# Kernel optimization log

Measured on AMD Instinct MI355X. Metric: run time of the kernel, lower is better.

## Reference

```python
import jax, jax.numpy as jnp
import numpy as np

# FP4 E2M1 magnitude lookup table (3-bit magnitude index)
FP4_LUT = jnp.array([0.0, 0.5, 1.0, 1.5, 2.0, 3.0, 4.0, 6.0], dtype=jnp.float32)
E8M0_BIAS = 127


def setup_inputs() -> dict:
    key = jax.random.key(0)
    k_in, k_pw, k_sc, k_b = jax.random.split(key, 4)
    B, S, I, O, BS = 4, 2048, 4096, 11008, 32
    inp = jax.random.normal(k_in, (B, S, I), dtype=jnp.float32)
    # packed MXFP4 codes: two 4-bit codes per byte
    packed_weight = jax.random.randint(k_pw, (O, I // 2), 0, 256, dtype=jnp.int32)
    # E8M0 exponents near the bias so dequantized magnitudes are O(1)
    weight_scales = jax.random.randint(k_sc, (O, I // BS), 118, 132, dtype=jnp.int32)
    bias = jax.random.normal(k_b, (O,), dtype=jnp.float32) * 0.02
    return {"input": inp, "bias": bias, "packed_weight": packed_weight,
            "weight_scales": weight_scales}


def _dequantize_mxfp4(packed_weight, weight_scales):
    O, P = packed_weight.shape
    I = P * 2
    bs = I // weight_scales.shape[1]
    lo = packed_weight & 0xF          # first element of each pair: low nibble
    hi = (packed_weight >> 4) & 0xF   # second element: high nibble
    codes = jnp.stack([lo, hi], axis=-1).reshape(O, I)  # [O, I]
    mag = FP4_LUT[codes & 0x7]
    sign = jnp.where((codes & 0x8) > 0, -1.0, 1.0)
    vals = sign * mag                                   # [O, I] fp4 values
    scale = jnp.exp2((weight_scales - E8M0_BIAS).astype(jnp.float32))  # [O, I/bs]
    w = (vals.reshape(O, I // bs, bs) * scale[:, :, None]).reshape(O, I)
    return w


def reference(input, bias, packed_weight, weight_scales):
    # quantized-inference path: on-the-fly block dequant + F.linear
    w = _dequantize_mxfp4(packed_weight, weight_scales)  # [O, I]
    out = jnp.einsum('bsi,oi->bso', input, w) + bias     # [B, S, O]
    return out
```

## Files before the change

kernel.cpp:

```cpp
#include <hip/hip_runtime.h>
#include <stdint.h>

typedef __attribute__((ext_vector_type(8))) short bf16x8;
typedef __attribute__((ext_vector_type(8))) unsigned short u16x8;
typedef __attribute__((ext_vector_type(4))) float f32x4;
typedef __attribute__((ext_vector_type(4))) int i32x4;

static constexpr int MDIM = 8192;
static constexpr int KDIM = 4096;
static constexpr int NDIM = 11008;
static constexpr int BM = 256, BN = 256, BK = 64;
static constexpr int NBX = NDIM / BN;
static constexpr int NBY = MDIM / BM;


static __device__ __forceinline__ unsigned short f2bf(float f) {
  unsigned int u = __builtin_bit_cast(unsigned int, f);
  return (unsigned short)((u + 0x7FFFu + ((u >> 16) & 1u)) >> 16);
}

static __device__ __forceinline__ float fp4_val(unsigned int c) {
  unsigned int m = c & 1u, e = (c >> 1) & 3u, s = (c >> 3) & 1u;
  unsigned int bits = e ? (((126u + e) << 23) | (m << 22)) : (m ? 0x3F000000u : 0u);
  bits |= s << 31;
  return __builtin_bit_cast(float, bits);
}

static constexpr int CONV_BLOCKS = (MDIM * KDIM / 8) / 256;
static constexpr int DEQ_BLOCKS  = (NDIM * (KDIM / 32)) / 256;

__global__ __launch_bounds__(256) void prep_kernel(
    const float4* __restrict__ in, u16x8* __restrict__ aout,
    const int* __restrict__ pw, const int* __restrict__ sc,
    unsigned short* __restrict__ wout) {
  if (blockIdx.x < CONV_BLOCKS) {
    int i = blockIdx.x * 256 + threadIdx.x;
    float4 v0 = in[2 * (size_t)i];
    float4 v1 = in[2 * (size_t)i + 1];
    u16x8 r;
    r[0] = f2bf(v0.x); r[1] = f2bf(v0.y); r[2] = f2bf(v0.z); r[3] = f2bf(v0.w);
    r[4] = f2bf(v1.x); r[5] = f2bf(v1.y); r[6] = f2bf(v1.z); r[7] = f2bf(v1.w);
    aout[i] = r;
  } else {
    int tid = (blockIdx.x - CONV_BLOCKS) * 256 + threadIdx.x;
    int o = tid >> 7;
    int b = tid & 127;
    const i32x4* src = (const i32x4*)(pw + (size_t)o * (KDIM / 2) + b * 16);
    unsigned int e = (unsigned int)sc[(size_t)o * (KDIM / 32) + b];
    float scale = __builtin_bit_cast(float, e << 23);
    unsigned short* dst = wout + (size_t)o * KDIM + b * 32;
#pragma unroll
    for (int v = 0; v < 4; ++v) {
      i32x4 w4 = src[v];
      u16x8 r;
#pragma unroll
      for (int j = 0; j < 4; ++j) {
        unsigned int w = (unsigned int)w4[j];
        r[2 * j]     = f2bf(fp4_val(w & 0xFu) * scale);
        r[2 * j + 1] = f2bf(fp4_val((w >> 4) & 0xFu) * scale);
      }
      *(u16x8*)(dst + 8 * v) = r;
    }
  }
}


#define GLDS16(gp, lp)                                                                  \
  __builtin_amdgcn_global_load_lds((const __attribute__((address_space(1))) void*)(gp), \
                                   (__attribute__((address_space(3))) void*)(lp), 16, 0, 0)

#define BAR() asm volatile("s_barrier" ::: "memory")

#define MFMA16(ACC, AV, BV, MO)                                                          \
  _Pragma("unroll") for (int m_ = 0; m_ < 4; ++m_)                                       \
  _Pragma("unroll") for (int n_ = 0; n_ < 4; ++n_)                                       \
      ACC[MO + m_][n_] = __builtin_amdgcn_mfma_f32_16x16x32_bf16(AV[m_], BV[n_],         \
                                                                 ACC[MO + m_][n_], 0, 0, 0)

template <int SLOT, bool STAGE>
__device__ __forceinline__ void ktile(
    unsigned char* lds, const unsigned short*& gA, const unsigned short*& gB,
    int stq, int aBase, int bBase, int kof0, int kof1, f32x4 (&acc)[8][4]) {
  const unsigned char* sa = lds + SLOT * 65536;
  const unsigned char* sb = sa + 32768;
  unsigned char* da = lds + (SLOT ^ 1) * 65536 + stq;
  unsigned char* db = da + 32768;
  bf16x8 a[4], b[4], a2[4];

#pragma unroll
  for (int m = 0; m < 4; ++m) a[m] = *(const bf16x8*)(sa + aBase + m * 2048 + kof0);
#pragma unroll
  for (int n = 0; n < 4; ++n) b[n] = *(const bf16x8*)(sb + bBase + n * 2048 + kof0);
  if (STAGE) {
    GLDS16(gB, db);
    GLDS16(gB + (size_t)64 * KDIM, db + 8192);
    asm volatile("s_waitcnt vmcnt(2)" ::: "memory");
  } else {
    asm volatile("s_waitcnt vmcnt(0)" ::: "memory");
  }
  BAR();
  __builtin_amdgcn_s_setprio(1);
  MFMA16(acc, a, b, 0);
  __builtin_amdgcn_s_setprio(0);
  BAR();

#pragma unroll
  for (int m = 0; m < 4; ++m) a2[m] = *(const bf16x8*)(sa + aBase + (4 + m) * 2048 + kof0);
  if (STAGE) {
    GLDS16(gB + (size_t)128 * KDIM, db + 16384);
    GLDS16(gB + (size_t)192 * KDIM, db + 24576);
  }
  BAR();
  __builtin_amdgcn_s_setprio(1);
  MFMA16(acc, a2, b, 4);
  __builtin_amdgcn_s_setprio(0);
  BAR();

#pragma unroll
  for (int m = 0; m < 4; ++m) a[m] = *(const bf16x8*)(sa + aBase + m * 2048 + kof1);
#pragma unroll
  for (int n = 0; n < 4; ++n) b[n] = *(const bf16x8*)(sb + bBase + n * 2048 + kof1);
  if (STAGE) {
    GLDS16(gA, da);
    GLDS16(gA + (size_t)128 * KDIM, da + 16384);
  }
  BAR();
  __builtin_amdgcn_s_setprio(1);
  MFMA16(acc, a, b, 0);
  __builtin_amdgcn_s_setprio(0);
  BAR();

#pragma unroll
  for (int m = 0; m < 4; ++m) a2[m] = *(const bf16x8*)(sa + aBase + (4 + m) * 2048 + kof1);
  if (STAGE) {
    GLDS16(gA + (size_t)64 * KDIM, da + 8192);
    GLDS16(gA + (size_t)192 * KDIM, da + 24576);
    gA += BK; gB += BK;
    asm volatile("s_waitcnt vmcnt(2)" ::: "memory");
  }
  BAR();
  __builtin_amdgcn_s_setprio(1);
  MFMA16(acc, a2, b, 4);
  __builtin_amdgcn_s_setprio(0);
  BAR();
}

__global__ __launch_bounds__(512, 2) void gemm_mx_kernel(
    const unsigned short* __restrict__ A,
    const unsigned short* __restrict__ Bw,
    const float* __restrict__ bias,
    float* __restrict__ C) {
  __shared__ __align__(16) unsigned char lds[2 * 65536];

  const int t = threadIdx.x;
  const int lane = t & 63;
  const int wave = t >> 6;
  const int wr = wave >> 2;
  const int wc = wave & 3;

  const int bid = blockIdx.x;
  const int swb = (bid & 7) * ((NBX * NBY) / 8) + (bid >> 3);
  const int by = swb / NBX;
  const int bx = swb - by * NBX;
  const int m0 = by * BM, n0 = bx * BN;

  const int fl = lane & 15;
  const int fh = lane >> 4;
  const int kof0 = ((fh)     ^ (fl & 7)) * 16;
  const int kof1 = ((4 + fh) ^ (fl & 7)) * 16;
  const int aBase = (wr * 128 + fl) * 128;
  const int bBase = (wc * 64 + fl) * 128;

  const int stq = t * 16;
  const int srow = t >> 3;
  const int koff = 8 * ((t & 7) ^ (srow & 7));
  const unsigned short* gA = A + (size_t)(m0 + srow) * KDIM + koff;
  const unsigned short* gB = Bw + (size_t)(n0 + srow) * KDIM + koff;

  f32x4 acc[8][4] = {};

  {
    unsigned char* da = lds + stq;
    unsigned char* db = da + 32768;
    GLDS16(gB, db);
    GLDS16(gB + (size_t)64 * KDIM, db + 8192);
    GLDS16(gB + (size_t)128 * KDIM, db + 16384);
    GLDS16(gB + (size_t)192 * KDIM, db + 24576);
    GLDS16(gA, da);
    GLDS16(gA + (size_t)128 * KDIM, da + 16384);
    GLDS16(gA + (size_t)64 * KDIM, da + 8192);
    GLDS16(gA + (size_t)192 * KDIM, da + 24576);
    gA += BK; gB += BK;
    asm volatile("s_waitcnt vmcnt(2)" ::: "memory");
    BAR();
  }

  for (int it = 0; it < 31; ++it) {
    ktile<0, true>(lds, gA, gB, stq, aBase, bBase, kof0, kof1, acc);
    ktile<1, true>(lds, gA, gB, stq, aBase, bBase, kof0, kof1, acc);
  }
  ktile<0, true>(lds, gA, gB, stq, aBase, bBase, kof0, kof1, acc);
  ktile<1, false>(lds, gA, gB, stq, aBase, bBase, kof0, kof1, acc);

#pragma unroll
  for (int n = 0; n < 4; ++n) {
    const int gn = n0 + wc * 64 + n * 16 + fl;
    const float bv = bias[gn];
#pragma unroll
    for (int m = 0; m < 8; ++m) {
      const int gm = m0 + wr * 128 + m * 16 + fh * 4;
      float* cp = C + (size_t)gm * NDIM + gn;
#pragma unroll
      for (int r = 0; r < 4; ++r)
        cp[(size_t)r * NDIM] = acc[m][n][r] + bv;
    }
  }
}

extern "C" void kernel_launch(void* const* d_in, const int* in_sizes, int n_in,
                              void* d_out, int out_size, void* d_ws, size_t ws_size,
                              hipStream_t stream) {
  const float* inp  = (const float*)d_in[0];
  const float* bias = (const float*)d_in[1];
  const int* pw     = (const int*)d_in[2];
  const int* sc     = (const int*)d_in[3];
  float* out = (float*)d_out;

  unsigned short* a_bf = (unsigned short*)d_ws;
  unsigned short* w_bf = a_bf + (size_t)MDIM * KDIM;
  size_t need = ((size_t)MDIM * KDIM + (size_t)NDIM * KDIM) * sizeof(unsigned short);
  if (ws_size < need) return;

  prep_kernel<<<dim3(CONV_BLOCKS + DEQ_BLOCKS), dim3(256), 0, stream>>>(
      (const float4*)inp, (u16x8*)a_bf, pw, sc, w_bf);
  gemm_mx_kernel<<<dim3(NBX * NBY), dim3(512), 0, stream>>>(a_bf, w_bf, bias, out);
}
```

Before: 859.7 us.

## Switch GEMM to 32x32x16 MFMA with 4-stage BK=32 LDS pipeline

Replaces the 16x16x32 bf16 MFMA tiling with 32x32x16 MFMAs, giving each wave a 4x2 grid of 32x32 accumulators. The K tile is halved to 32 and the LDS is split into four 32 KB slots, so three tiles are in flight through global_load_lds with a counted vmcnt wait. Each k-tile now needs one barrier instead of several. This aims to cut barrier overhead and hide global-memory latency better. In exchange it adds more pipeline stages with shorter compute per stage and a new swizzle and epilogue mapping that must stay correct.

```diff
diff --git a/kernel.cpp b/kernel.cpp
--- a/kernel.cpp
+++ b/kernel.cpp
@@ -3,13 +3,13 @@
 
 typedef __attribute__((ext_vector_type(8))) short bf16x8;
 typedef __attribute__((ext_vector_type(8))) unsigned short u16x8;
-typedef __attribute__((ext_vector_type(4))) float f32x4;
+typedef __attribute__((ext_vector_type(16))) float f32x16;
 typedef __attribute__((ext_vector_type(4))) int i32x4;
 
 static constexpr int MDIM = 8192;
 static constexpr int KDIM = 4096;
 static constexpr int NDIM = 11008;
-static constexpr int BM = 256, BN = 256, BK = 64;
+static constexpr int BM = 256, BN = 256, BK = 32;
 static constexpr int NBX = NDIM / BN;
 static constexpr int NBY = MDIM / BM;
 
@@ -71,78 +71,47 @@
 
 #define BAR() asm volatile("s_barrier" ::: "memory")
 
-#define MFMA16(ACC, AV, BV, MO)                                                          \
-  _Pragma("unroll") for (int m_ = 0; m_ < 4; ++m_)                                       \
-  _Pragma("unroll") for (int n_ = 0; n_ < 4; ++n_)                                       \
-      ACC[MO + m_][n_] = __builtin_amdgcn_mfma_f32_16x16x32_bf16(AV[m_], BV[n_],         \
-                                                                 ACC[MO + m_][n_], 0, 0, 0)
-
-template <int SLOT, bool STAGE>
+template <int SLOT, bool STAGE, int VN>
 __device__ __forceinline__ void ktile(
     unsigned char* lds, const unsigned short*& gA, const unsigned short*& gB,
-    int stq, int aBase, int bBase, int kof0, int kof1, f32x4 (&acc)[8][4]) {
-  const unsigned char* sa = lds + SLOT * 65536;
-  const unsigned char* sb = sa + 32768;
-  unsigned char* da = lds + (SLOT ^ 1) * 65536 + stq;
-  unsigned char* db = da + 32768;
-  bf16x8 a[4], b[4], a2[4];
-
-#pragma unroll
-  for (int m = 0; m < 4; ++m) a[m] = *(const bf16x8*)(sa + aBase + m * 2048 + kof0);
-#pragma unroll
-  for (int n = 0; n < 4; ++n) b[n] = *(const bf16x8*)(sb + bBase + n * 2048 + kof0);
+    int stq, int aBase, int bBase, int kof0, int kof1, f32x16 (&acc)[4][2]) {
+  if constexpr (VN == 8)      asm volatile("s_waitcnt vmcnt(8)" ::: "memory");
+  else if constexpr (VN == 4) asm volatile("s_waitcnt vmcnt(4)" ::: "memory");
+  else                        asm volatile("s_waitcnt vmcnt(0)" ::: "memory");
+  BAR();
   if (STAGE) {
-    GLDS16(gB, db);
-    GLDS16(gB + (size_t)64 * KDIM, db + 8192);
-    asm volatile("s_waitcnt vmcnt(2)" ::: "memory");
-  } else {
-    asm volatile("s_waitcnt vmcnt(0)" ::: "memory");
-  }
-  BAR();
+    unsigned char* da = lds + ((SLOT + 3) & 3) * 32768 + stq;
+    GLDS16(gA, da);
+    GLDS16(gA + (size_t)128 * KDIM, da + 8192);
+    GLDS16(gB, da + 16384);
+    GLDS16(gB + (size_t)128 * KDIM, da + 24576);
+    gA += BK; gB += BK;
+  }
+  const unsigned char* sa = lds + SLOT * 32768;
+  const unsigned char* sb = sa + 16384;
+  bf16x8 a[4], b[2];
+#pragma unroll
+  for (int mf = 0; mf < 4; ++mf) a[mf] = *(const bf16x8*)(sa + aBase + mf * 2048 + kof0);
+#pragma unroll
+  for (int nf = 0; nf < 2; ++nf) b[nf] = *(const bf16x8*)(sb + bBase + nf * 2048 + kof0);
   __builtin_amdgcn_s_setprio(1);
-  MFMA16(acc, a, b, 0);
+#pragma unroll
+  for (int mf = 0; mf < 4; ++mf)
+#pragma unroll
+    for (int nf = 0; nf < 2; ++nf)
+      acc[mf][nf] = __builtin_amdgcn_mfma_f32_32x32x16_bf16(a[mf], b[nf], acc[mf][nf], 0, 0, 0);
   __builtin_amdgcn_s_setprio(0);
-  BAR();
-
-#pragma unroll
-  for (int m = 0; m < 4; ++m) a2[m] = *(const bf16x8*)(sa + aBase + (4 + m) * 2048 + kof0);
-  if (STAGE) {
-    GLDS16(gB + (size_t)128 * KDIM, db + 16384);
-    GLDS16(gB + (size_t)192 * KDIM, db + 24576);
-  }
-  BAR();
+#pragma unroll
+  for (int mf = 0; mf < 4; ++mf) a[mf] = *(const bf16x8*)(sa + aBase + mf * 2048 + kof1);
+#pragma unroll
+  for (int nf = 0; nf < 2; ++nf) b[nf] = *(const bf16x8*)(sb + bBase + nf * 2048 + kof1);
   __builtin_amdgcn_s_setprio(1);
-  MFMA16(acc, a2, b, 4);
+#pragma unroll
+  for (int mf = 0; mf < 4; ++mf)
+#pragma unroll
+    for (int nf = 0; nf < 2; ++nf)
+      acc[mf][nf] = __builtin_amdgcn_mfma_f32_32x32x16_bf16(a[mf], b[nf], acc[mf][nf], 0, 0, 0);
   __builtin_amdgcn_s_setprio(0);
-  BAR();
-
-#pragma unroll
-  for (int m = 0; m < 4; ++m) a[m] = *(const bf16x8*)(sa + aBase + m * 2048 + kof1);
-#pragma unroll
-  for (int n = 0; n < 4; ++n) b[n] = *(const bf16x8*)(sb + bBase + n * 2048 + kof1);
-  if (STAGE) {
-    GLDS16(gA, da);
-    GLDS16(gA + (size_t)128 * KDIM, da + 16384);
-  }
-  BAR();
-  __builtin_amdgcn_s_setprio(1);
-  MFMA16(acc, a, b, 0);
-  __builtin_amdgcn_s_setprio(0);
-  BAR();
-
-#pragma unroll
-  for (int m = 0; m < 4; ++m) a2[m] = *(const bf16x8*)(sa + aBase + (4 + m) * 2048 + kof1);
-  if (STAGE) {
-    GLDS16(gA + (size_t)64 * KDIM, da + 8192);
-    GLDS16(gA + (size_t)192 * KDIM, da + 24576);
-    gA += BK; gB += BK;
-    asm volatile("s_waitcnt vmcnt(2)" ::: "memory");
-  }
-  BAR();
-  __builtin_amdgcn_s_setprio(1);
-  MFMA16(acc, a2, b, 4);
-  __builtin_amdgcn_s_setprio(0);
-  BAR();
 }
 
 __global__ __launch_bounds__(512, 2) void gemm_mx_kernel(
@@ -150,7 +119,7 @@
     const unsigned short* __restrict__ Bw,
     const float* __restrict__ bias,
     float* __restrict__ C) {
-  __shared__ __align__(16) unsigned char lds[2 * 65536];
+  __shared__ __align__(16) unsigned char lds[4 * 32768];
 
   const int t = threadIdx.x;
   const int lane = t & 63;
@@ -164,55 +133,56 @@
   const int bx = swb - by * NBX;
   const int m0 = by * BM, n0 = bx * BN;
 
-  const int fl = lane & 15;
-  const int fh = lane >> 4;
-  const int kof0 = ((fh)     ^ (fl & 7)) * 16;
-  const int kof1 = ((4 + fh) ^ (fl & 7)) * 16;
-  const int aBase = (wr * 128 + fl) * 128;
-  const int bBase = (wc * 64 + fl) * 128;
+  const int rl = lane & 31;
+  const int hi = lane >> 5;
+  const int kof0 = ((2 * 0 + hi) ^ (rl & 3)) * 16;
+  const int kof1 = ((2 * 1 + hi) ^ (rl & 3)) * 16;
+  const int aBase = (wr * 128 + rl) * 64;
+  const int bBase = (wc * 64 + rl) * 64;
 
   const int stq = t * 16;
-  const int srow = t >> 3;
-  const int koff = 8 * ((t & 7) ^ (srow & 7));
+  const int srow = t >> 2;
+  const int koff = 8 * ((t & 3) ^ (srow & 3));
   const unsigned short* gA = A + (size_t)(m0 + srow) * KDIM + koff;
   const unsigned short* gB = Bw + (size_t)(n0 + srow) * KDIM + koff;
 
-  f32x4 acc[8][4] = {};
-
-  {
-    unsigned char* da = lds + stq;
-    unsigned char* db = da + 32768;
-    GLDS16(gB, db);
-    GLDS16(gB + (size_t)64 * KDIM, db + 8192);
-    GLDS16(gB + (size_t)128 * KDIM, db + 16384);
-    GLDS16(gB + (size_t)192 * KDIM, db + 24576);
+  f32x16 acc[4][2] = {};
+
+#pragma unroll
+  for (int p = 0; p < 3; ++p) {
+    unsigned char* da = lds + p * 32768 + stq;
     GLDS16(gA, da);
-    GLDS16(gA + (size_t)128 * KDIM, da + 16384);
-    GLDS16(gA + (size_t)64 * KDIM, da + 8192);
-    GLDS16(gA + (size_t)192 * KDIM, da + 24576);
+    GLDS16(gA + (size_t)128 * KDIM, da + 8192);
+    GLDS16(gB, da + 16384);
+    GLDS16(gB + (size_t)128 * KDIM, da + 24576);
     gA += BK; gB += BK;
-    asm volatile("s_waitcnt vmcnt(2)" ::: "memory");
-    BAR();
   }
 
   for (int it = 0; it < 31; ++it) {
-    ktile<0, true>(lds, gA, gB, stq, aBase, bBase, kof0, kof1, acc);
-    ktile<1, true>(lds, gA, gB, stq, aBase, bBase, kof0, kof1, acc);
-  }
-  ktile<0, true>(lds, gA, gB, stq, aBase, bBase, kof0, kof1, acc);
-  ktile<1, false>(lds, gA, gB, stq, aBase, bBase, kof0, kof1, acc);
-
-#pragma unroll
-  for (int n = 0; n < 4; ++n) {
-    const int gn = n0 + wc * 64 + n * 16 + fl;
+    ktile<0, true, 8>(lds, gA, gB, stq, aBase, bBase, kof0, kof1, acc);
+    ktile<1, true, 8>(lds, gA, gB, stq, aBase, bBase, kof0, kof1, acc);
+    ktile<2, true, 8>(lds, gA, gB, stq, aBase, bBase, kof0, kof1, acc);
+    ktile<3, true, 8>(lds, gA, gB, stq, aBase, bBase, kof0, kof1, acc);
+  }
+  ktile<0, true, 8>(lds, gA, gB, stq, aBase, bBase, kof0, kof1, acc);
+  ktile<1, false, 8>(lds, gA, gB, stq, aBase, bBase, kof0, kof1, acc);
+  ktile<2, false, 4>(lds, gA, gB, stq, aBase, bBase, kof0, kof1, acc);
+  ktile<3, false, 0>(lds, gA, gB, stq, aBase, bBase, kof0, kof1, acc);
+
+#pragma unroll
+  for (int nf = 0; nf < 2; ++nf) {
+    const int gn = n0 + wc * 64 + nf * 32 + rl;
     const float bv = bias[gn];
 #pragma unroll
-    for (int m = 0; m < 8; ++m) {
-      const int gm = m0 + wr * 128 + m * 16 + fh * 4;
-      float* cp = C + (size_t)gm * NDIM + gn;
-#pragma unroll
-      for (int r = 0; r < 4; ++r)
-        cp[(size_t)r * NDIM] = acc[m][n][r] + bv;
+    for (int mf = 0; mf < 4; ++mf) {
+      const int base = m0 + wr * 128 + mf * 32 + 4 * hi;
+#pragma unroll
+      for (int q = 0; q < 4; ++q) {
+        float* cp = C + (size_t)(base + 8 * q) * NDIM + gn;
+#pragma unroll
+        for (int rr = 0; rr < 4; ++rr)
+          cp[(size_t)rr * NDIM] = acc[mf][nf][q * 4 + rr] + bv;
+      }
     }
   }
 }
```

Measured after the change: 906.0 us. 1.05x slower.
